# Performance work log

Measured on AMD Instinct MI355X. Metric: run time of the kernel, lower is better.

Reference implementation:

```python
import jax, jax.numpy as jnp
import numpy as np

NEG_INF = -1e9
H = 512  # hidden_size


def _glorot(key, shape):
    lim = np.sqrt(6.0 / (shape[0] + shape[1])).astype(np.float32)
    return jax.random.uniform(key, shape, jnp.float32, -lim, lim)


def _lstm_bias():
    b = np.zeros(4 * H, dtype=np.float32)
    b[H:2 * H] = 1.0  # forget-gate bias = 1
    return jnp.asarray(b)


def setup_inputs() -> dict:
    key = jax.random.key(0)
    ks = jax.random.split(key, 14)
    B, T_SRC, T_TGT = 64, 512, 256
    inp = {
        "tgt_token_embeddings": jax.random.normal(ks[0], (B, T_TGT, H), jnp.float32),
        "fw_h": jax.random.normal(ks[1], (B, H), jnp.float32) * 0.1,
        "fw_c": jax.random.normal(ks[2], (B, H), jnp.float32) * 0.1,
        "bw_h": jax.random.normal(ks[3], (B, H), jnp.float32) * 0.1,
        "bw_c": jax.random.normal(ks[4], (B, H), jnp.float32) * 0.1,
        "encoder_outputs": jax.random.normal(ks[5], (B, T_SRC, 2 * H), jnp.float32),
        "padding_mask": jax.random.randint(ks[6], (B, T_SRC), 0, 2).astype(jnp.float32),
        # Luong attention params
        "W_memory": _glorot(ks[7], (2 * H, H)),
        "W_attention": _glorot(ks[8], (3 * H, H)),
        # stacked 2-layer LSTM params; layer 1 input = concat(embed, attn) -> 2H
        "ki1": _glorot(ks[9], (2 * H, 4 * H)),
        "kr1": _glorot(ks[10], (H, 4 * H)),
        "b1": _lstm_bias(),
        "ki2": _glorot(ks[11], (H, 4 * H)),
        "kr2": _glorot(ks[12], (H, 4 * H)),
        "b2": _lstm_bias(),
    }
    return inp


def _lstm_step(x, h, c, ki, kr, b):
    # gate order i, f, j, o (j = candidate), matching the TF cell
    z = x @ ki + h @ kr + b
    i, f, j, o = jnp.split(z, 4, axis=1)
    c = jax.nn.sigmoid(f) * c + jax.nn.sigmoid(i) * jnp.tanh(j)
    h = jax.nn.sigmoid(o) * jnp.tanh(c)
    return h, c


def reference(tgt_token_embeddings, fw_h, fw_c, bw_h, bw_c, encoder_outputs,
              padding_mask, W_memory, W_attention, ki1, kr1, b1, ki2, kr2, b2):
    B = tgt_token_embeddings.shape[0]
    # memory projection is time-invariant: hoist out of the scan
    ref_mem = jnp.einsum('bsk,kh->bsh', encoder_outputs, W_memory)  # [B,S,H]
    mask_add = padding_mask * NEG_INF  # [B,S]

    def step(carry, x_t):
        h1, c1, h2, c2, attn = carry
        x = jnp.concatenate([x_t, attn], axis=1)            # [B,2H]
        h1, c1 = _lstm_step(x, h1, c1, ki1, kr1, b1)
        h2, c2 = _lstm_step(h1, h2, c2, ki2, kr2, b2)
        # Luong attention: query = h2
        scores = jnp.einsum('bsh,bh->bs', ref_mem, h2) + mask_add
        w = jax.nn.softmax(scores, axis=1)                  # [B,S]
        context = jnp.einsum('bs,bsk->bk', w, encoder_outputs)  # [B,2H]
        attn = jnp.concatenate([h2, context], axis=1) @ W_attention  # [B,H]
        return (h1, c1, h2, c2, attn), attn

    attn0 = jnp.zeros((B, H), jnp.float32)
    carry0 = (fw_h, fw_c, bw_h, bw_c, attn0)
    _, outs = jax.lax.scan(step, carry0, jnp.swapaxes(tgt_token_embeddings, 0, 1))
    return jnp.swapaxes(outs, 0, 1)  # [B, T_tgt, H]
```

## Files before the change

kernel.cpp:

```cpp
#include <hip/hip_runtime.h>
#include <stdint.h>


typedef float f32x4 __attribute__((ext_vector_type(4)));

struct Params {
  const float* tgtT4;
  const float* mask;
  const float* b1;
  const float* b2;
  const float* Wm;
  const float* enc;
  const float* W1T;
  const float* W2T;
  const float* WaT;
  float *h1a,*h1b,*h2a,*h2b;
  float *attnT4;
  float *q;
  float *c1,*c2;
  float *eh2;
  float *part_ctx;
  float *part_ml;
  uint64_t *pktab;
  int      *natab;
  float *out;
};

__device__ __forceinline__ float sigmf(float x){ return 1.f/(1.f+__expf(-x)); }

template<int NCOLS, int KGW, int KST>
__device__ __forceinline__ void mm_core(const float* seg0, const float* seg1, const float* seg2,
                                        const float* wL, float* zb, int lane, int wv){
  float acc[NCOLS];
  #pragma unroll
  for (int c=0;c<NCOLS;++c) acc[c]=0.f;
  const int kg0 = wv*KGW;
  #pragma unroll 4
  for (int i=0;i<KGW;++i){
    const int kg = kg0 + i;
    const float* bp = (kg<128) ? seg0 : ((kg<256) ? seg1 : seg2);
    f32x4 a = *(const f32x4*)(bp + ((size_t)kg<<8) + (lane<<2));
    #pragma unroll
    for (int c=0;c<NCOLS;++c){
      f32x4 w = *(const f32x4*)(wL + c*KST + (kg<<2));
      acc[c] = fmaf(a[0],w[0],acc[c]); acc[c] = fmaf(a[1],w[1],acc[c]);
      acc[c] = fmaf(a[2],w[2],acc[c]); acc[c] = fmaf(a[3],w[3],acc[c]);
    }
  }
  #pragma unroll
  for (int c=0;c<NCOLS;++c) zb[(wv*NCOLS+c)*64 + lane] = acc[c];
}

template<int PHASE>
__global__ __launch_bounds__(512, 2)
void k_lstm(Params P, int t, int rp){
  constexpr int KF  = (PHASE==1) ? 1536 : 1024;
  constexpr int KGW = (PHASE==1) ? 48 : 32;
  constexpr int KQ  = KF/4;
  __shared__ float smem[8*KF + 4096 + 512];
  float* zb = smem + 8*KF;
  float* zs = zb + 4096;
  const int wg=blockIdx.x, tid=threadIdx.x, lane=tid&63, wv=tid>>6;
  const float* WT = (PHASE==1) ? P.W1T : P.W2T;
  #pragma unroll
  for (int c=0;c<8;++c){
    const int n = ((c>>1)<<9) + (wg<<1) + (c&1);
    const f32x4* src = (const f32x4*)(WT + (size_t)n*KF);
    f32x4* dst = (f32x4*)(smem + c*KF);
    if (tid < KQ) dst[tid] = src[tid];
  }
  __syncthreads();

  const float* h1r = rp ? P.h1b : P.h1a;
  float*       h1w = rp ? P.h1a : P.h1b;
  const float* h2r = rp ? P.h2b : P.h2a;
  float*       h2w = rp ? P.h2a : P.h2b;

  if (PHASE==1){
    const float* seg0 = P.tgtT4 + ((size_t)t<<15);
    const float* seg1 = P.attnT4 - 32768;
    const float* seg2 = h1r - 65536;
    mm_core<8,KGW,KF>(seg0, seg1, seg2, smem, zb, lane, wv);
  } else {
    const float* seg0 = h1w;
    const float* seg1 = h2r - 32768;
    mm_core<8,KGW,KF>(seg0, seg1, seg1, smem, zb, lane, wv);
  }
  __syncthreads();
  {
    const int gc = tid>>6, b = tid&63;
    float s = 0.f;
    #pragma unroll
    for (int w=0; w<8; ++w) s += zb[(w*8+gc)*64 + b];
    zs[gc*64 + b] = s;
  }
  __syncthreads();
  if (tid < 128){
    const int b = tid&63, j = tid>>6;
    const int h = (wg<<1)+j;
    const float* bias = (PHASE==1) ? P.b1 : P.b2;
    float z[4];
    #pragma unroll
    for (int g=0; g<4; ++g) z[g] = zs[(g*2+j)*64 + b] + bias[(g<<9)+h];
    float* cb = (PHASE==1) ? P.c1 : P.c2;
    float* hw = (PHASE==1) ? h1w  : h2w;
    const int ci = (b<<9)+h;
    float co = cb[ci];
    float cn = sigmf(z[1])*co + sigmf(z[0])*tanhf(z[2]);
    float hn = sigmf(z[3])*tanhf(cn);
    cb[ci] = cn;
    hw[((h>>2)<<8) + (b<<2) + (h&3)] = hn;
  }
}

__global__ __launch_bounds__(512, 2)
void k_qproj(Params P, int rp){
  __shared__ float smem[2048 + 1024 + 3072];
  float* wm = smem;
  float* wa = smem + 2048;
  float* zb = smem + 3072;
  const int wg=blockIdx.x, tid=threadIdx.x, lane=tid&63, wv=tid>>6;
  {
    const int c = tid>>7, qi = tid&127;
    const f32x4* src = (const f32x4*)(P.Wm + (size_t)((wg<<2)+c)*512);
    ((f32x4*)wm)[tid] = src[qi];
  }
  if (tid < 256){
    const int c = tid>>7, qi = tid&127;
    const f32x4* src = (const f32x4*)(P.WaT + (size_t)((wg<<1)+c)*1536);
    ((f32x4*)wa)[tid] = src[qi];
  }
  __syncthreads();
  const float* h2n = rp ? P.h2a : P.h2b;
  float accq[4] = {0.f,0.f,0.f,0.f};
  float acce[2] = {0.f,0.f};
  const int kg0 = wv*16;
  #pragma unroll 4
  for (int i=0;i<16;++i){
    const int kg = kg0 + i;
    f32x4 a = *(const f32x4*)(h2n + ((size_t)kg<<8) + (lane<<2));
    #pragma unroll
    for (int c=0;c<4;++c){
      f32x4 w = *(const f32x4*)(wm + c*512 + (kg<<2));
      accq[c] = fmaf(a[0],w[0],accq[c]); accq[c] = fmaf(a[1],w[1],accq[c]);
      accq[c] = fmaf(a[2],w[2],accq[c]); accq[c] = fmaf(a[3],w[3],accq[c]);
    }
    #pragma unroll
    for (int c=0;c<2;++c){
      f32x4 w = *(const f32x4*)(wa + c*512 + (kg<<2));
      acce[c] = fmaf(a[0],w[0],acce[c]); acce[c] = fmaf(a[1],w[1],acce[c]);
      acce[c] = fmaf(a[2],w[2],acce[c]); acce[c] = fmaf(a[3],w[3],acce[c]);
    }
  }
  #pragma unroll
  for (int c=0;c<4;++c) zb[(wv*6+c)*64 + lane] = accq[c];
  #pragma unroll
  for (int c=0;c<2;++c) zb[(wv*6+4+c)*64 + lane] = acce[c];
  __syncthreads();
  if (tid < 384){
    const int b = tid&63, gc = tid>>6;
    float s = 0.f;
    #pragma unroll
    for (int w=0; w<8; ++w) s += zb[(w*6+gc)*64 + b];
    if (gc < 4) P.q[(b<<10) + (wg<<2) + gc] = s;
    else        P.eh2[(b<<9) + (wg<<1) + (gc-4)] = s;
  }
}

struct Row { f32x4 v[4]; };
__device__ __forceinline__ Row load_row(const float* ep, int r){
  Row c;
  const float* p = ep + ((size_t)r<<10);
  c.v[0]=*(const f32x4*)p;     c.v[1]=*(const f32x4*)(p+4);
  c.v[2]=*(const f32x4*)(p+8); c.v[3]=*(const f32x4*)(p+12);
  return c;
}

__global__ __launch_bounds__(512, 2)
void k_attn(Params P, int rp){
  __shared__ float cpart[4*1024];
  __shared__ float ml[16];
  const int wg=blockIdx.x, tid=threadIdx.x, lane=tid&63, wv=tid>>6;
  const int b = wg>>2, sg = wg&3;
  const int s0 = (sg<<7) + (wv<<4);
  const float* ep = P.enc + (((size_t)b*512 + s0)<<10) + (lane<<4);
  const uint64_t pk = P.pktab[(size_t)wg*8 + wv];
  const int    nact = P.natab[(size_t)wg*8 + wv];
  const float* qp = P.q + (b<<10) + (lane<<4);
  f32x4 qv0=*(const f32x4*)qp,     qv1=*(const f32x4*)(qp+4),
        qv2=*(const f32x4*)(qp+8), qv3=*(const f32x4*)(qp+12);
  float m=-1e30f, l=0.f;
  f32x4 cx0={0,0,0,0}, cx1={0,0,0,0}, cx2={0,0,0,0}, cx3={0,0,0,0};
  Row cur = load_row(ep, (int)(pk & 15));
  #pragma clang loop unroll(disable)
  for (int i=0;i<nact;++i){
    Row nxt;
    if (i+1<nact) nxt = load_row(ep, (int)((pk>>(4*(i+1)))&15));
    float d=0.f;
    #pragma unroll
    for (int j=0;j<4;++j){
      d=fmaf(cur.v[0][j],qv0[j],d); d=fmaf(cur.v[1][j],qv1[j],d);
      d=fmaf(cur.v[2][j],qv2[j],d); d=fmaf(cur.v[3][j],qv3[j],d);
    }
    d += __shfl_xor(d,1,64);  d += __shfl_xor(d,2,64);  d += __shfl_xor(d,4,64);
    d += __shfl_xor(d,8,64);  d += __shfl_xor(d,16,64); d += __shfl_xor(d,32,64);
    float mn = fmaxf(m, d);
    float fs = __expf(m - mn), e_ = __expf(d - mn);
    l = l*fs + e_;
    cx0 = cx0*fs + cur.v[0]*e_;  cx1 = cx1*fs + cur.v[1]*e_;
    cx2 = cx2*fs + cur.v[2]*e_;  cx3 = cx3*fs + cur.v[3]*e_;
    m = mn;
    cur = nxt;
  }
  if (wv < 4){
    float* cp = cpart + (wv<<10) + (lane<<2);
    *(f32x4*)(cp      ) = cx0; *(f32x4*)(cp + 256) = cx1;
    *(f32x4*)(cp + 512) = cx2; *(f32x4*)(cp + 768) = cx3;
  }
  if (lane==0){ ml[wv*2]=m; ml[wv*2+1]=l; }
  __syncthreads();
  if (wv >= 4){
    float M = -1e30f;
    #pragma unroll
    for (int w=0;w<8;++w) M = fmaxf(M, ml[w*2]);
    const float ewj = __expf(ml[(wv-4)*2]-M);
    const float ewo = __expf(ml[wv*2]-M);
    float* cp = cpart + ((wv-4)<<10) + (lane<<2);
    f32x4 r0=*(f32x4*)(cp), r1=*(f32x4*)(cp+256), r2=*(f32x4*)(cp+512), r3=*(f32x4*)(cp+768);
    r0 = r0*ewj + cx0*ewo;  r1 = r1*ewj + cx1*ewo;
    r2 = r2*ewj + cx2*ewo;  r3 = r3*ewj + cx3*ewo;
    *(f32x4*)(cp) = r0; *(f32x4*)(cp+256)=r1; *(f32x4*)(cp+512)=r2; *(f32x4*)(cp+768)=r3;
    if (wv==4 && lane==0){
      float L = 0.f;
      #pragma unroll
      for (int w=0;w<8;++w) L += __expf(ml[w*2]-M)*ml[w*2+1];
      P.part_ml[b*8 + sg*2]   = M;
      P.part_ml[b*8 + sg*2+1] = L;
    }
  }
  __syncthreads();
  #pragma unroll
  for (int h=0; h<2; ++h){
    const int f = tid + (h<<9);
    const int fidx = (((f&15)>>2)<<8) + ((f>>4)<<2) + (f&3);
    float c = 0.f;
    #pragma unroll
    for (int p=0;p<4;++p) c += cpart[(p<<10) + fidx];
    P.part_ctx[((size_t)sg<<16) + ((f>>2)<<8) + (b<<2) + (f&3)] = c;
  }
}

__global__ __launch_bounds__(512, 2)
void k_out(Params P, int t, int rp){
  __shared__ float smem[2048 + 1024];
  float* wa = smem;
  float* zb = smem + 2048;
  const int wg=blockIdx.x, tid=threadIdx.x, lane=tid&63, wv=tid>>6;
  {
    const int c = tid>>8, qi = tid&255;
    const f32x4* src = (const f32x4*)(P.WaT + (size_t)((wg<<1)+c)*1536 + 512);
    ((f32x4*)wa)[tid] = src[qi];
  }
  __syncthreads();
  f32x4 mlv0 = *(const f32x4*)(P.part_ml + lane*8);
  f32x4 mlv1 = *(const f32x4*)(P.part_ml + lane*8 + 4);
  float M0=mlv0[0], L0=mlv0[1], M1=mlv0[2], L1=mlv0[3];
  float M2=mlv1[0], L2=mlv1[1], M3=mlv1[2], L3=mlv1[3];
  float M = fmaxf(fmaxf(M0,M1), fmaxf(M2,M3));
  float w0=__expf(M0-M), w1=__expf(M1-M), w2=__expf(M2-M), w3=__expf(M3-M);
  float inv = 1.f/(w0*L0 + w1*L1 + w2*L2 + w3*L3);
  w0*=inv; w1*=inv; w2*=inv; w3*=inv;

  float acc0=0.f, acc1=0.f;
  const int kk0 = wv*32;
  #pragma unroll 2
  for (int i=0;i<32;++i){
    const int kk = kk0 + i;
    const float* pc = P.part_ctx + ((size_t)kk<<8) + (lane<<2);
    f32x4 g0 = *(const f32x4*)pc;
    f32x4 g1 = *(const f32x4*)(pc + 65536);
    f32x4 g2 = *(const f32x4*)(pc + 131072);
    f32x4 g3 = *(const f32x4*)(pc + 196608);
    f32x4 a;
    #pragma unroll
    for (int j=0;j<4;++j) a[j] = w0*g0[j] + w1*g1[j] + w2*g2[j] + w3*g3[j];
    f32x4 u0 = *(const f32x4*)(wa + (kk<<2));
    f32x4 u1 = *(const f32x4*)(wa + 1024 + (kk<<2));
    acc0 = fmaf(a[0],u0[0],acc0); acc0 = fmaf(a[1],u0[1],acc0);
    acc0 = fmaf(a[2],u0[2],acc0); acc0 = fmaf(a[3],u0[3],acc0);
    acc1 = fmaf(a[0],u1[0],acc1); acc1 = fmaf(a[1],u1[1],acc1);
    acc1 = fmaf(a[2],u1[2],acc1); acc1 = fmaf(a[3],u1[3],acc1);
  }
  zb[(wv*2+0)*64 + lane] = acc0;
  zb[(wv*2+1)*64 + lane] = acc1;
  __syncthreads();
  if (tid < 128){
    const int b = tid&63, j = tid>>6;
    const int n = (wg<<1)+j;
    float s = P.eh2[(b<<9) + n];
    #pragma unroll
    for (int w=0;w<8;++w) s += zb[(w*2+j)*64 + b];
    P.out[(((size_t)b<<8) + t)*512 + n] = s;
    P.attnT4[((n>>2)<<8) + (b<<2) + (n&3)] = s;
  }
}

__global__ void transT(const float* a, const float* bsrc, float* dst, int K, int N, int KA){
  __shared__ float tile[32][33];
  const int ntk = K>>5;
  const int tn = blockIdx.x / ntk, tk = blockIdx.x - tn*ntk;
  const int tid = threadIdx.x;
  const int c = tid & 31, r = tid >> 5;
  for (int rr=r; rr<32; rr+=8){
    const int k = (tk<<5)+rr, n = (tn<<5)+c;
    tile[rr][c] = (k<KA) ? a[(size_t)k*N+n] : bsrc[(size_t)(k-KA)*N+n];
  }
  __syncthreads();
  for (int rr=r; rr<32; rr+=8){
    const int n = (tn<<5)+rr, k = (tk<<5)+c;
    dst[(size_t)n*K + k] = tile[c][rr];
  }
}

__global__ void prep_tgt(const float* tgt, float* tgtT4){
  __shared__ float xt[64*517];
  const int t = blockIdx.x, tid = threadIdx.x;
  for (int i=tid; i<64*512; i+=256){
    const int bb = i>>9, k = i&511;
    xt[bb*517 + k] = tgt[((size_t)bb*256 + t)*512 + k];
  }
  __syncthreads();
  for (int i=tid; i<128*64; i+=256){
    const int kg = i>>6, bb = i&63;
    f32x4 v = { xt[bb*517 + kg*4], xt[bb*517 + kg*4 + 1],
                xt[bb*517 + kg*4 + 2], xt[bb*517 + kg*4 + 3] };
    *(f32x4*)(tgtT4 + ((size_t)t<<15) + (kg<<8) + (bb<<2)) = v;
  }
}

__global__ void prep_pk(const float* mask, uint64_t* pktab, int* natab){
  const int e = blockIdx.x*blockDim.x + threadIdx.x;
  if (e >= 2048) return;
  const int wv = e & 7, sg = (e>>3) & 3, b = e>>5;
  const int s0 = (sg<<7) + (wv<<4);
  uint64_t pk = 0; int nact = 0;
  for (int r=0;r<16;++r){
    if (mask[(b<<9) + s0 + r] == 0.f){ pk |= (uint64_t)r << (4*nact); ++nact; }
  }
  pktab[((size_t)(b*4+sg))*8 + wv] = pk;
  natab[((size_t)(b*4+sg))*8 + wv] = nact;
}

__global__ void init_state(const float* fwh, const float* fwc, const float* bwh, const float* bwc,
                           float* h1a, float* h2a, float* attnT4, float* c1, float* c2){
  const int i = blockIdx.x*blockDim.x + threadIdx.x;
  if (i < 64*512){
    const int bb = i>>9, k = i&511;
    const int t4 = ((k>>2)<<8) + (bb<<2) + (k&3);
    h1a[t4] = fwh[i];
    h2a[t4] = bwh[i];
    attnT4[t4] = 0.f;
    c1[i] = fwc[i];
    c2[i] = bwc[i];
  }
}

extern "C" void kernel_launch(void* const* d_in, const int* in_sizes, int n_in,
                              void* d_out, int out_size, void* d_ws, size_t ws_size,
                              hipStream_t stream){
  if (n_in < 15) return;
  const float* tgt = (const float*)d_in[0];
  const float* fwh = (const float*)d_in[1];
  const float* fwc = (const float*)d_in[2];
  const float* bwh = (const float*)d_in[3];
  const float* bwc = (const float*)d_in[4];
  const float* enc = (const float*)d_in[5];
  const float* msk = (const float*)d_in[6];
  const float* Wm  = (const float*)d_in[7];
  const float* Wa  = (const float*)d_in[8];
  const float* ki1 = (const float*)d_in[9];
  const float* kr1 = (const float*)d_in[10];
  const float* b1  = (const float*)d_in[11];
  const float* ki2 = (const float*)d_in[12];
  const float* kr2 = (const float*)d_in[13];
  const float* b2  = (const float*)d_in[14];

  char* w = (char*)d_ws;
  size_t o = 0;
  auto carve = [&](size_t bytes)->char*{
    char* r = w + o; o = (o + bytes + 255) & ~(size_t)255; return r;
  };
  float* W1T    = (float*)carve(2048ull*1536*4);
  float* W2T    = (float*)carve(2048ull*1024*4);
  float* WaT    = (float*)carve(512ull*1536*4);
  float* tgtT4  = (float*)carve(256ull*128*256*4);
  float* h1a    = (float*)carve(128ull*256*4);
  float* h1b    = (float*)carve(128ull*256*4);
  float* h2a    = (float*)carve(128ull*256*4);
  float* h2b    = (float*)carve(128ull*256*4);
  float* attnT4 = (float*)carve(128ull*256*4);
  float* q      = (float*)carve(64ull*1024*4);
  float* c1     = (float*)carve(64ull*512*4);
  float* c2     = (float*)carve(64ull*512*4);
  float* eh2    = (float*)carve(64ull*512*4);
  float* part_ctx = (float*)carve(4ull*256*256*4);
  float* part_ml  = (float*)carve(64ull*8*4);
  uint64_t* pktab = (uint64_t*)carve(2048ull*8);
  int*      natab = (int*)carve(2048ull*4);
  if (o > ws_size) return;

  hipLaunchKernelGGL(transT, dim3(64*48), dim3(256), 0, stream, ki1, kr1, W1T, 1536, 2048, 1024);
  hipLaunchKernelGGL(transT, dim3(64*32), dim3(256), 0, stream, ki2, kr2, W2T, 1024, 2048, 512);
  hipLaunchKernelGGL(transT, dim3(16*48), dim3(256), 0, stream, Wa,  Wa,  WaT, 1536, 512, 1536);
  hipLaunchKernelGGL(prep_tgt, dim3(256), dim3(256), 0, stream, tgt, tgtT4);
  hipLaunchKernelGGL(prep_pk,  dim3(8),   dim3(256), 0, stream, msk, pktab, natab);
  hipLaunchKernelGGL(init_state, dim3(128), dim3(256), 0, stream,
                     fwh, fwc, bwh, bwc, h1a, h2a, attnT4, c1, c2);

  Params P;
  P.tgtT4 = tgtT4; P.mask = msk; P.b1 = b1; P.b2 = b2;
  P.Wm = Wm; P.enc = enc;
  P.W1T = W1T; P.W2T = W2T; P.WaT = WaT;
  P.h1a = h1a; P.h1b = h1b; P.h2a = h2a; P.h2b = h2b;
  P.attnT4 = attnT4; P.q = q;
  P.c1 = c1; P.c2 = c2; P.eh2 = eh2;
  P.part_ctx = part_ctx; P.part_ml = part_ml;
  P.pktab = pktab; P.natab = natab;
  P.out = (float*)d_out;

  for (int t = 0; t < 256; ++t){
    const int rp = t & 1;
    hipLaunchKernelGGL(k_lstm<1>, dim3(256), dim3(512), 0, stream, P, t, rp);
    hipLaunchKernelGGL(k_lstm<2>, dim3(256), dim3(512), 0, stream, P, t, rp);
    hipLaunchKernelGGL(k_qproj,   dim3(256), dim3(512), 0, stream, P, rp);
    hipLaunchKernelGGL(k_attn,    dim3(256), dim3(512), 0, stream, P, rp);
    hipLaunchKernelGGL(k_out,     dim3(256), dim3(512), 0, stream, P, t, rp);
  }
}
```

Before: 18.38 ms.

## Split attention over 8 source segments per batch and deepen row prefetch

The attention kernel now uses 512 workgroups, 8 per batch row, each wave covering 8 source positions instead of 16. The goal is to raise parallelism and occupancy across the 256 CUs, with launch bounds raised to 4 blocks per CU. The row loads are double-prefetched two iterations ahead. In exchange, the output kernel must merge 8 partial contexts and 8 (max, sum) pairs per batch instead of 4, which doubles partial-context traffic and adds work to k_out.

```diff
diff --git a/kernel.cpp b/kernel.cpp
--- a/kernel.cpp
+++ b/kernel.cpp
@@ -21,7 +21,7 @@
   float *eh2;
   float *part_ctx;
   float *part_ml;
-  uint64_t *pktab;
+  uint32_t *pktab;
   int      *natab;
   float *out;
 };
@@ -176,26 +176,29 @@
   return c;
 }
 
-__global__ __launch_bounds__(512, 2)
+__global__ __launch_bounds__(512, 4)
 void k_attn(Params P, int rp){
   __shared__ float cpart[4*1024];
   __shared__ float ml[16];
   const int wg=blockIdx.x, tid=threadIdx.x, lane=tid&63, wv=tid>>6;
-  const int b = wg>>2, sg = wg&3;
-  const int s0 = (sg<<7) + (wv<<4);
+  const int b = wg>>3, sg = wg&7;
+  const int s0 = (sg<<6) + (wv<<3);
   const float* ep = P.enc + (((size_t)b*512 + s0)<<10) + (lane<<4);
-  const uint64_t pk = P.pktab[(size_t)wg*8 + wv];
+  const uint32_t pk = P.pktab[(size_t)wg*8 + wv];
   const int    nact = P.natab[(size_t)wg*8 + wv];
   const float* qp = P.q + (b<<10) + (lane<<4);
   f32x4 qv0=*(const f32x4*)qp,     qv1=*(const f32x4*)(qp+4),
         qv2=*(const f32x4*)(qp+8), qv3=*(const f32x4*)(qp+12);
   float m=-1e30f, l=0.f;
   f32x4 cx0={0,0,0,0}, cx1={0,0,0,0}, cx2={0,0,0,0}, cx3={0,0,0,0};
-  Row cur = load_row(ep, (int)(pk & 15));
+  Row r0, r1;
+  if (nact > 0) r0 = load_row(ep, (int)(pk & 15));
+  if (nact > 1) r1 = load_row(ep, (int)((pk>>4) & 15));
   #pragma clang loop unroll(disable)
   for (int i=0;i<nact;++i){
-    Row nxt;
-    if (i+1<nact) nxt = load_row(ep, (int)((pk>>(4*(i+1)))&15));
+    Row cur = r0;
+    r0 = r1;
+    if (i+2 < nact) r1 = load_row(ep, (int)((pk>>(4*(i+2)))&15));
     float d=0.f;
     #pragma unroll
     for (int j=0;j<4;++j){
@@ -210,7 +213,6 @@
     cx0 = cx0*fs + cur.v[0]*e_;  cx1 = cx1*fs + cur.v[1]*e_;
     cx2 = cx2*fs + cur.v[2]*e_;  cx3 = cx3*fs + cur.v[3]*e_;
     m = mn;
-    cur = nxt;
   }
   if (wv < 4){
     float* cp = cpart + (wv<<10) + (lane<<2);
@@ -226,16 +228,16 @@
     const float ewj = __expf(ml[(wv-4)*2]-M);
     const float ewo = __expf(ml[wv*2]-M);
     float* cp = cpart + ((wv-4)<<10) + (lane<<2);
-    f32x4 r0=*(f32x4*)(cp), r1=*(f32x4*)(cp+256), r2=*(f32x4*)(cp+512), r3=*(f32x4*)(cp+768);
-    r0 = r0*ewj + cx0*ewo;  r1 = r1*ewj + cx1*ewo;
-    r2 = r2*ewj + cx2*ewo;  r3 = r3*ewj + cx3*ewo;
-    *(f32x4*)(cp) = r0; *(f32x4*)(cp+256)=r1; *(f32x4*)(cp+512)=r2; *(f32x4*)(cp+768)=r3;
+    f32x4 q0=*(f32x4*)(cp), q1=*(f32x4*)(cp+256), q2=*(f32x4*)(cp+512), q3=*(f32x4*)(cp+768);
+    q0 = q0*ewj + cx0*ewo;  q1 = q1*ewj + cx1*ewo;
+    q2 = q2*ewj + cx2*ewo;  q3 = q3*ewj + cx3*ewo;
+    *(f32x4*)(cp) = q0; *(f32x4*)(cp+256)=q1; *(f32x4*)(cp+512)=q2; *(f32x4*)(cp+768)=q3;
     if (wv==4 && lane==0){
       float L = 0.f;
       #pragma unroll
       for (int w=0;w<8;++w) L += __expf(ml[w*2]-M)*ml[w*2+1];
-      P.part_ml[b*8 + sg*2]   = M;
-      P.part_ml[b*8 + sg*2+1] = L;
+      P.part_ml[b*16 + sg*2]   = M;
+      P.part_ml[b*16 + sg*2+1] = L;
     }
   }
   __syncthreads();
@@ -262,14 +264,21 @@
     ((f32x4*)wa)[tid] = src[qi];
   }
   __syncthreads();
-  f32x4 mlv0 = *(const f32x4*)(P.part_ml + lane*8);
-  f32x4 mlv1 = *(const f32x4*)(P.part_ml + lane*8 + 4);
-  float M0=mlv0[0], L0=mlv0[1], M1=mlv0[2], L1=mlv0[3];
-  float M2=mlv1[0], L2=mlv1[1], M3=mlv1[2], L3=mlv1[3];
-  float M = fmaxf(fmaxf(M0,M1), fmaxf(M2,M3));
-  float w0=__expf(M0-M), w1=__expf(M1-M), w2=__expf(M2-M), w3=__expf(M3-M);
-  float inv = 1.f/(w0*L0 + w1*L1 + w2*L2 + w3*L3);
-  w0*=inv; w1*=inv; w2*=inv; w3*=inv;
+  f32x4 mlv0 = *(const f32x4*)(P.part_ml + lane*16);
+  f32x4 mlv1 = *(const f32x4*)(P.part_ml + lane*16 + 4);
+  f32x4 mlv2 = *(const f32x4*)(P.part_ml + lane*16 + 8);
+  f32x4 mlv3 = *(const f32x4*)(P.part_ml + lane*16 + 12);
+  float Ms[8] = {mlv0[0],mlv0[2],mlv1[0],mlv1[2],mlv2[0],mlv2[2],mlv3[0],mlv3[2]};
+  float Ls[8] = {mlv0[1],mlv0[3],mlv1[1],mlv1[3],mlv2[1],mlv2[3],mlv3[1],mlv3[3]};
+  float M = -1e30f;
+  #pragma unroll
+  for (int s=0;s<8;++s) M = fmaxf(M, Ms[s]);
+  float ws[8]; float L = 0.f;
+  #pragma unroll
+  for (int s=0;s<8;++s){ ws[s] = __expf(Ms[s]-M); L += ws[s]*Ls[s]; }
+  float inv = 1.f/L;
+  #pragma unroll
+  for (int s=0;s<8;++s) ws[s] *= inv;
 
   float acc0=0.f, acc1=0.f;
   const int kk0 = wv*32;
@@ -277,13 +286,13 @@
   for (int i=0;i<32;++i){
     const int kk = kk0 + i;
     const float* pc = P.part_ctx + ((size_t)kk<<8) + (lane<<2);
-    f32x4 g0 = *(const f32x4*)pc;
-    f32x4 g1 = *(const f32x4*)(pc + 65536);
-    f32x4 g2 = *(const f32x4*)(pc + 131072);
-    f32x4 g3 = *(const f32x4*)(pc + 196608);
-    f32x4 a;
-    #pragma unroll
-    for (int j=0;j<4;++j) a[j] = w0*g0[j] + w1*g1[j] + w2*g2[j] + w3*g3[j];
+    f32x4 a = {0.f,0.f,0.f,0.f};
+    #pragma unroll
+    for (int s=0;s<8;++s){
+      f32x4 g = *(const f32x4*)(pc + (size_t)s*65536);
+      a[0] = fmaf(ws[s],g[0],a[0]); a[1] = fmaf(ws[s],g[1],a[1]);
+      a[2] = fmaf(ws[s],g[2],a[2]); a[3] = fmaf(ws[s],g[3],a[3]);
+    }
     f32x4 u0 = *(const f32x4*)(wa + (kk<<2));
     f32x4 u1 = *(const f32x4*)(wa + 1024 + (kk<<2));
     acc0 = fmaf(a[0],u0[0],acc0); acc0 = fmaf(a[1],u0[1],acc0);
@@ -338,17 +347,17 @@
   }
 }
 
-__global__ void prep_pk(const float* mask, uint64_t* pktab, int* natab){
+__global__ void prep_pk(const float* mask, uint32_t* pktab, int* natab){
   const int e = blockIdx.x*blockDim.x + threadIdx.x;
-  if (e >= 2048) return;
-  const int wv = e & 7, sg = (e>>3) & 3, b = e>>5;
-  const int s0 = (sg<<7) + (wv<<4);
-  uint64_t pk = 0; int nact = 0;
-  for (int r=0;r<16;++r){
-    if (mask[(b<<9) + s0 + r] == 0.f){ pk |= (uint64_t)r << (4*nact); ++nact; }
-  }
-  pktab[((size_t)(b*4+sg))*8 + wv] = pk;
-  natab[((size_t)(b*4+sg))*8 + wv] = nact;
+  if (e >= 4096) return;
+  const int wv = e & 7, sg = (e>>3) & 7, b = e>>6;
+  const int s0 = (sg<<6) + (wv<<3);
+  uint32_t pk = 0; int nact = 0;
+  for (int r=0;r<8;++r){
+    if (mask[(b<<9) + s0 + r] == 0.f){ pk |= (uint32_t)r << (4*nact); ++nact; }
+  }
+  pktab[((size_t)(b*8+sg))*8 + wv] = pk;
+  natab[((size_t)(b*8+sg))*8 + wv] = nact;
 }
 
 __global__ void init_state(const float* fwh, const float* fwc, const float* bwh, const float* bwc,
@@ -403,17 +412,17 @@
   float* c1     = (float*)carve(64ull*512*4);
   float* c2     = (float*)carve(64ull*512*4);
   float* eh2    = (float*)carve(64ull*512*4);
-  float* part_ctx = (float*)carve(4ull*256*256*4);
-  float* part_ml  = (float*)carve(64ull*8*4);
-  uint64_t* pktab = (uint64_t*)carve(2048ull*8);
-  int*      natab = (int*)carve(2048ull*4);
+  float* part_ctx = (float*)carve(8ull*256*256*4);
+  float* part_ml  = (float*)carve(64ull*16*4);
+  uint32_t* pktab = (uint32_t*)carve(4096ull*4);
+  int*      natab = (int*)carve(4096ull*4);
   if (o > ws_size) return;
 
   hipLaunchKernelGGL(transT, dim3(64*48), dim3(256), 0, stream, ki1, kr1, W1T, 1536, 2048, 1024);
   hipLaunchKernelGGL(transT, dim3(64*32), dim3(256), 0, stream, ki2, kr2, W2T, 1024, 2048, 512);
   hipLaunchKernelGGL(transT, dim3(16*48), dim3(256), 0, stream, Wa,  Wa,  WaT, 1536, 512, 1536);
   hipLaunchKernelGGL(prep_tgt, dim3(256), dim3(256), 0, stream, tgt, tgtT4);
-  hipLaunchKernelGGL(prep_pk,  dim3(8),   dim3(256), 0, stream, msk, pktab, natab);
+  hipLaunchKernelGGL(prep_pk,  dim3(16),  dim3(256), 0, stream, msk, pktab, natab);
   hipLaunchKernelGGL(init_state, dim3(128), dim3(256), 0, stream,
                      fwh, fwc, bwh, bwc, h1a, h2a, attnT4, c1, c2);
 
@@ -433,7 +442,7 @@
     hipLaunchKernelGGL(k_lstm<1>, dim3(256), dim3(512), 0, stream, P, t, rp);
     hipLaunchKernelGGL(k_lstm<2>, dim3(256), dim3(512), 0, stream, P, t, rp);
     hipLaunchKernelGGL(k_qproj,   dim3(256), dim3(512), 0, stream, P, rp);
-    hipLaunchKernelGGL(k_attn,    dim3(256), dim3(512), 0, stream, P, rp);
+    hipLaunchKernelGGL(k_attn,    dim3(512), dim3(512), 0, stream, P, rp);
     hipLaunchKernelGGL(k_out,     dim3(256), dim3(512), 0, stream, P, t, rp);
   }
 }
```

Result: slower. 23.18 ms (+26.1%).
